# Kernel optimization log

Hardware: AMD Instinct MI355X
Metric: run time of the kernel (lower is better)

Reference implementation:

```python
import jax, jax.numpy as jnp
import numpy as np

B, N_PER_G, DEG = 128, 1024, 8
N = B * N_PER_G
E = N * DEG
IN_DIM, HID, OUT_DIM = 128, 64, 10
EPS = 1e-5


def _gcn(x, src, dst, ew, W, b, n_nodes):
    # GCNConv with add_self_loops=True, symmetric normalization, edge weights ew in {0,1}
    xw = x @ W                                                 # [N, HID]
    deg = jax.ops.segment_sum(ew, dst, num_segments=n_nodes) + 1.0  # +1 self loop
    dinv = jax.lax.rsqrt(deg)
    norm = dinv[src] * dinv[dst] * ew                          # [E]
    agg = jax.ops.segment_sum(xw[src] * norm[:, None], dst, num_segments=n_nodes)
    return agg + xw * (dinv * dinv)[:, None] + b               # self-loop term + bias


def _bn_relu(x, g, beta):
    # BatchNorm1d training-mode stats over node dim (biased var), then ReLU
    mu = x.mean(0)
    var = ((x - mu) ** 2).mean(0)
    return jax.nn.relu((x - mu) * jax.lax.rsqrt(var + EPS) * g + beta)


def _topk_pool(x, src, dst, ew, p, n_per_g):
    # PyG TopKPooling: score = x.p/||p||, keep top ceil(0.8*n) per graph, x *= tanh(score)
    k = (4 * n_per_g + 4) // 5  # ceil(0.8 * n), static
    score = (x @ p) / jnp.linalg.norm(p)                       # [B*n]
    _, idx = jax.lax.top_k(score.reshape(B, n_per_g), k)       # [B, k] local indices
    perm = (idx + (jnp.arange(B) * n_per_g)[:, None]).reshape(-1)  # [B*k] global
    xs = x[perm] * jnp.tanh(score[perm])[:, None]
    # re-index edges; edges touching dropped nodes get weight 0 (mask, fixed E)
    mapping = jnp.full((B * n_per_g,), -1, jnp.int32).at[perm].set(
        jnp.arange(B * k, dtype=jnp.int32))
    ns, nd = mapping[src], mapping[dst]
    valid = (ns >= 0) & (nd >= 0) & (ew > 0)
    return xs, jnp.where(valid, ns, 0), jnp.where(valid, nd, 0), valid.astype(x.dtype), k


def _readout(x, k):
    xg = x.reshape(B, k, HID)
    return jnp.concatenate([xg.mean(1), xg.max(1)], axis=1)    # [B, 2*HID]


def _forward(x, edge_index, W1, b1, gamma1, beta1, p1, W2, b2, gamma2, beta2, p2,
             W3, b3, gamma3, beta3, p3, Wm, bm):
    src, dst = edge_index[0], edge_index[1]
    ew = jnp.ones((E,), x.dtype)
    n = N_PER_G
    blocks = [(W1, b1, gamma1, beta1, p1),
              (W2, b2, gamma2, beta2, p2),
              (W3, b3, gamma3, beta3, p3)]
    readout = jnp.zeros((B, 2 * HID), x.dtype)
    for W, b, g, bt, p in blocks:
        h = _gcn(x, src, dst, ew, W, b, B * n)
        h = _bn_relu(h, g, bt)
        x, src, dst, ew, n = _topk_pool(h, src, dst, ew, p, n)
        readout = readout + _readout(x, n)
    return readout @ Wm + bm                                   # [B, OUT_DIM]


def setup_inputs():
    key = jax.random.key(0)
    ks = jax.random.split(key, 20)
    x = jax.random.normal(ks[0], (N, IN_DIM), jnp.float32)
    src_l = jax.random.randint(ks[1], (E,), 0, N_PER_G)
    dst_l = jax.random.randint(ks[2], (E,), 0, N_PER_G)
    off = jnp.repeat(jnp.arange(B, dtype=jnp.int32) * N_PER_G, N_PER_G * DEG)
    edge_index = jnp.stack([src_l.astype(jnp.int32) + off,
                            dst_l.astype(jnp.int32) + off])   # [2, E] intra-graph
    d = {"x": x, "edge_index": edge_index}
    dims = [(IN_DIM, HID), (HID, HID), (HID, HID)]
    for i, (di, do) in enumerate(dims, 1):
        d[f"W{i}"] = jax.random.normal(ks[3 * i], (di, do), jnp.float32) / np.sqrt(di)
        d[f"b{i}"] = jnp.zeros((do,), jnp.float32)
        d[f"gamma{i}"] = jnp.ones((do,), jnp.float32)
        d[f"beta{i}"] = jnp.zeros((do,), jnp.float32)
        d[f"p{i}"] = jax.random.normal(ks[3 * i + 1], (do,), jnp.float32)
    d["Wm"] = jax.random.normal(ks[15], (2 * HID, OUT_DIM), jnp.float32) / np.sqrt(2 * HID)
    d["bm"] = jnp.zeros((OUT_DIM,), jnp.float32)
    return d


def reference(x, edge_index, W1, b1, gamma1, beta1, p1, W2, b2, gamma2, beta2, p2,
              W3, b3, gamma3, beta3, p3, Wm, bm):
    return _forward(x, edge_index, W1, b1, gamma1, beta1, p1,
                    W2, b2, gamma2, beta2, p2, W3, b3, gamma3, beta3, p3, Wm, bm)
```

## Files before the change

### kernel.cpp

```cpp
#include <hip/hip_runtime.h>
#include <cmath>
#include <cstdint>
#include <cstddef>

#define HID 64
#define NGR 128
#define NTOT 131072
#define EDGES 1048576
#define EPG 8192

__global__ __launch_bounds__(256) void pack_init(
    const int* __restrict__ ei, uint32_t* __restrict__ packed,
    uint16_t* __restrict__ csr_g, uint32_t* __restrict__ rs_g,
    float* __restrict__ dinv_g, float* __restrict__ sums3,
    float* __restrict__ readout) {
  __shared__ int hist[1024];
  __shared__ int part[256];
  __shared__ int cursor[1024];
  int b = blockIdx.x, t = threadIdx.x;
  for (int i = t; i < 1024; i += 256) hist[i] = 0;
  __syncthreads();
  int ebase = b * EPG, nbase = b << 10;
  for (int e = t; e < EPG; e += 256) {
    uint32_t s = (uint32_t)(ei[ebase + e] - nbase);
    uint32_t d = (uint32_t)(ei[EDGES + ebase + e] - nbase);
    packed[ebase + e] = s | (d << 10);
    atomicAdd(&hist[(int)d], 1);
  }
  __syncthreads();
  int h0 = hist[t * 4], h1 = hist[t * 4 + 1], h2 = hist[t * 4 + 2], h3 = hist[t * 4 + 3];
  int tot = h0 + h1 + h2 + h3;
  part[t] = tot;
  __syncthreads();
  for (int off = 1; off < 256; off <<= 1) {
    int v = (t >= off) ? part[t - off] : 0;
    __syncthreads();
    part[t] += v;
    __syncthreads();
  }
  int excl = part[t] - tot;
  int r0 = excl, r1 = r0 + h0, r2 = r1 + h1, r3 = r2 + h2;
  cursor[t * 4 + 0] = r0; cursor[t * 4 + 1] = r1;
  cursor[t * 4 + 2] = r2; cursor[t * 4 + 3] = r3;
  uint32_t* rg = rs_g + b * 1025;
  rg[t * 4 + 0] = r0; rg[t * 4 + 1] = r1; rg[t * 4 + 2] = r2; rg[t * 4 + 3] = r3;
  if (t == 255) rg[1024] = EPG;
  for (int i = t; i < 1024; i += 256)
    dinv_g[(b << 10) + i] = rsqrtf((float)hist[i] + 1.0f);
  __syncthreads();
  for (int e = t; e < EPG; e += 256) {
    uint32_t pk = packed[ebase + e];
    int d = (pk >> 10) & 1023;
    int idx = atomicAdd(&cursor[d], 1);
    csr_g[ebase + idx] = (uint16_t)(pk & 1023);
  }
  if (b < 3 && t < 128) sums3[b * 128 + t] = 0.0f;
  if (t < 128) readout[b * 128 + t] = 0.0f;
}

template<int DIN, bool TIN>
__global__ __launch_bounds__(256) void gemm_xw(
    const float* __restrict__ X, const float* __restrict__ W,
    float* __restrict__ XWT, int n_nodes) {
  __shared__ float sW[32 * HID];
  __shared__ float sX[32 * 132];
  const int t = threadIdx.x;
  const int cq = t & 15, ng = t >> 4;
  const int c4 = cq * 4;
  const int node0 = blockIdx.x * 128;
  const size_t Nn = (size_t)n_nodes;
  float acc[8][4];
#pragma unroll
  for (int n = 0; n < 8; n++) { acc[n][0]=0.f; acc[n][1]=0.f; acc[n][2]=0.f; acc[n][3]=0.f; }

  for (int k0 = 0; k0 < DIN; k0 += 32) {
    ((float4*)sW)[t * 2 + 0] = ((const float4*)(W + (size_t)k0 * HID))[t * 2 + 0];
    ((float4*)sW)[t * 2 + 1] = ((const float4*)(W + (size_t)k0 * HID))[t * 2 + 1];
    if (TIN) {
#pragma unroll
      for (int it = 0; it < 4; it++) {
        int slot = t + it * 256;
        int row = slot >> 5, col4 = (slot & 31) * 4;
        *(float4*)(sX + row * 132 + col4) =
            *(const float4*)(X + (size_t)(k0 + row) * Nn + node0 + col4);
      }
    } else {
      int i4 = (t & 7) * 4;
      int nl = t >> 3;
#pragma unroll
      for (int rep = 0; rep < 4; rep++) {
        int nn = nl + rep * 32;
        float4 v = *(const float4*)(X + (size_t)(node0 + nn) * DIN + k0 + i4);
        sX[(i4 + 0) * 132 + nn] = v.x;
        sX[(i4 + 1) * 132 + nn] = v.y;
        sX[(i4 + 2) * 132 + nn] = v.z;
        sX[(i4 + 3) * 132 + nn] = v.w;
      }
    }
    __syncthreads();
#pragma unroll 4
    for (int i = 0; i < 32; i++) {
      float4 w = *(const float4*)(sW + i * HID + c4);
      const float* xr = sX + i * 132 + ng * 8;
      float4 xa = *(const float4*)xr;
      float4 xb = *(const float4*)(xr + 4);
      float xn[8] = {xa.x, xa.y, xa.z, xa.w, xb.x, xb.y, xb.z, xb.w};
#pragma unroll
      for (int n = 0; n < 8; n++) {
        acc[n][0] = fmaf(xn[n], w.x, acc[n][0]);
        acc[n][1] = fmaf(xn[n], w.y, acc[n][1]);
        acc[n][2] = fmaf(xn[n], w.z, acc[n][2]);
        acc[n][3] = fmaf(xn[n], w.w, acc[n][3]);
      }
    }
    __syncthreads();
  }
#pragma unroll
  for (int cc = 0; cc < 4; cc++) {
    int row = c4 + cc;
    float* o = XWT + (size_t)row * Nn + node0 + ng * 8;
    *(float4*)(o + 0) = make_float4(acc[0][cc], acc[1][cc], acc[2][cc], acc[3][cc]);
    *(float4*)(o + 4) = make_float4(acc[4][cc], acc[5][cc], acc[6][cc], acc[7][cc]);
  }
}

__global__ __launch_bounds__(1024, 8) void edge_agg(
    const uint16_t* __restrict__ csr_g, const uint32_t* __restrict__ rs_g,
    const float* __restrict__ dinv_g, const float* __restrict__ xwT,
    const float* __restrict__ bias, float* __restrict__ hT,
    float* __restrict__ sums) {
  __shared__ float xws[8 * 1028];
  __shared__ float dv[1024];
  __shared__ uint32_t rs[1025];
  __shared__ uint16_t csr_s[8192];
  __shared__ float sredS[16][8], sredQ[16][8];
  const int g = blockIdx.x & 127;
  const int q = blockIdx.x >> 7;
  const int c0 = q * 8;
  const int t = threadIdx.x;
  const int gbase = g << 10;

  dv[t] = dinv_g[gbase + t];
  if (t < 1024) rs[t] = rs_g[g * 1025 + t];
  if (t == 0) rs[1024] = EPG;
  ((uint4*)csr_s)[t] = ((const uint4*)(csr_g + (size_t)g * EPG))[t];
  for (int slot = t; slot < 2048; slot += 1024) {
    int c = slot >> 8, pos4 = (slot & 255) * 4;
    float4 v = *(const float4*)(xwT + (size_t)(c0 + c) * NTOT + gbase + pos4);
    float4 dd = *(const float4*)(dinv_g + gbase + pos4);
    v.x *= dd.x; v.y *= dd.y; v.z *= dd.z; v.w *= dd.w;
    *(float4*)(xws + c * 1028 + pos4) = v;
  }
  __syncthreads();

  const int c = t & 7, j = t >> 3;
  const float* xc = xws + c * 1028;
  const float bv = bias[c0 + c];
  float* hrow = hT + (size_t)(c0 + c) * NTOT + gbase;
  float S = 0.0f, Q = 0.0f;
  for (int d = j; d < 1024; d += 128) {
    float dvd = dv[d];
    if (dvd == 0.0f) continue;
    int e = rs[d], e1 = rs[d + 1];
    float a0 = 0.0f, a1 = 0.0f;
    for (; e + 2 <= e1; e += 2) {
      int s0 = csr_s[e], s1 = csr_s[e + 1];
      a0 += xc[s0];
      a1 += xc[s1];
    }
    if (e < e1) a0 += xc[csr_s[e]];
    float hv = (a0 + a1 + xc[d]) * dvd + bv;
    hrow[d] = hv;
    S += hv; Q += hv * hv;
  }
#pragma unroll
  for (int m = 8; m < 64; m <<= 1) { S += __shfl_xor(S, m); Q += __shfl_xor(Q, m); }
  {
    int lane = t & 63, w = t >> 6;
    if (lane < 8) { sredS[w][lane] = S; sredQ[w][lane] = Q; }
  }
  __syncthreads();
  if (t < 8) {
    float a = 0.0f;
    for (int w2 = 0; w2 < 16; w2++) a += sredS[w2][t];
    atomicAdd(&sums[c0 + t], a);
  } else if (t < 16) {
    int cc = t - 8;
    float a = 0.0f;
    for (int w2 = 0; w2 < 16; w2++) a += sredQ[w2][cc];
    atomicAdd(&sums[64 + cc + c0], a);
  }
}

__global__ __launch_bounds__(256) void score_kernel(
    const float* __restrict__ hT, const float* __restrict__ sums,
    const float* __restrict__ gamma, const float* __restrict__ beta,
    const float* __restrict__ p, const float* __restrict__ dinv_g,
    float* __restrict__ score, float* __restrict__ stanh_g, float inv_n) {
  __shared__ float ssc[64], ssh[64], sp[64];
  __shared__ float sipn;
  int b = blockIdx.x >> 2, seg = (blockIdx.x & 3) << 8;
  int t = threadIdx.x;
  int node = (b << 10) + seg + t;
  if (t < 64) {
    float mu = sums[t] * inv_n;
    float var = fmaxf(sums[64 + t] * inv_n - mu * mu, 0.0f);
    float sc = rsqrtf(var + 1e-5f) * gamma[t];
    ssc[t] = sc; ssh[t] = beta[t] - mu * sc;
    sp[t] = p[t];
  }
  __syncthreads();
  if (t == 0) {
    float s = 0.0f;
    for (int i = 0; i < 64; i++) s += sp[i] * sp[i];
    sipn = rsqrtf(s);
  }
  __syncthreads();
  const float* hp = hT + node;
  float s0 = 0.0f;
#pragma unroll 16
  for (int c = 0; c < 64; c++) {
    float y = fmaxf(fmaf(hp[(size_t)c * NTOT], ssc[c], ssh[c]), 0.0f);
    s0 = fmaf(y, sp[c], s0);
  }
  float v0 = s0 * sipn;
  score[node] = (dinv_g[node] > 0.0f) ? v0 : -INFINITY;
  stanh_g[node] = tanhf(v0);
}

__global__ __launch_bounds__(1024) void topk_kernel(
    const float* __restrict__ score, const uint32_t* __restrict__ packed,
    float* __restrict__ dinv_g, int* __restrict__ snext_g, int k, int hasNext) {
  __shared__ float __align__(16) ssc[1024];
  __shared__ int snext[1024];
  __shared__ int shist[1024];
  int b = blockIdx.x, t = threadIdx.x;
  int gbase = b << 10;
  ssc[t] = score[gbase + t];
  shist[t] = 0;
  __syncthreads();
  float my = ssc[t];
  int r = 0;
  for (int jb = 0; jb < 256; jb++) {
    float4 v = ((const float4*)ssc)[jb];
    int j0 = jb * 4;
    r += (v.x > my) || (v.x == my && (j0 + 0) < t);
    r += (v.y > my) || (v.y == my && (j0 + 1) < t);
    r += (v.z > my) || (v.z == my && (j0 + 2) < t);
    r += (v.w > my) || (v.w == my && (j0 + 3) < t);
  }
  int kept = (r < k) ? 1 : 0;
  snext[t] = kept;
  snext_g[gbase + t] = kept;
  __syncthreads();
  if (hasNext) {
    const uint32_t* pe = packed + (size_t)b * EPG;
#pragma unroll
    for (int e0 = 0; e0 < EPG; e0 += 1024) {
      uint32_t pk = pe[e0 + t];
      int s = pk & 1023, d = (pk >> 10) & 1023;
      if (snext[s] & snext[d]) atomicAdd(&shist[d], 1);
    }
    __syncthreads();
    dinv_g[gbase + t] = kept ? rsqrtf((float)shist[t] + 1.0f) : 0.0f;
  }
}

__global__ __launch_bounds__(256) void pool_kernel(
    const float* __restrict__ hT, const float* __restrict__ sums,
    const float* __restrict__ gamma, const float* __restrict__ beta,
    const float* __restrict__ stanh_g, const int* __restrict__ snext_g,
    float* __restrict__ xT_out, float* __restrict__ readout,
    int k, float inv_n) {
  __shared__ float ssc[64], ssh[64];
  __shared__ float sth[1024];
  __shared__ int skn[1024];
  __shared__ float redS[4][8], redM[4][8];
  int g = blockIdx.x & 127, q = blockIdx.x >> 7;
  int t = threadIdx.x;
  int gbase = g << 10;
  if (t < 64) {
    float mu = sums[t] * inv_n;
    float var = fmaxf(sums[64 + t] * inv_n - mu * mu, 0.0f);
    float sc = rsqrtf(var + 1e-5f) * gamma[t];
    ssc[t] = sc; ssh[t] = beta[t] - mu * sc;
  }
  for (int i = t; i < 1024; i += 256) {
    sth[i] = stanh_g[gbase + i];
    skn[i] = snext_g[gbase + i];
  }
  __syncthreads();
  int lane = t & 63, w = t >> 6;
#pragma unroll
  for (int i = 0; i < 8; i++) {
    int c = q * 8 + i;
    const float* hrow = hT + (size_t)c * NTOT + gbase;
    float* xrow = xT_out ? (xT_out + (size_t)c * NTOT + gbase) : nullptr;
    float scc = ssc[c], shh = ssh[c];
    float S = 0.0f, M = -INFINITY;
    for (int nd = t; nd < 1024; nd += 256) {
      bool kn = skn[nd] != 0;
      float y = fmaxf(fmaf(hrow[nd], scc, shh), 0.0f) * sth[nd];
      y = kn ? y : 0.0f;
      if (xrow) xrow[nd] = y;
      S += y;
      if (kn) M = fmaxf(M, y);
    }
#pragma unroll
    for (int m = 1; m < 64; m <<= 1) {
      S += __shfl_xor(S, m);
      M = fmaxf(M, __shfl_xor(M, m));
    }
    if (lane == 0) { redS[w][i] = S; redM[w][i] = M; }
  }
  __syncthreads();
  if (t < 8) {
    float S = redS[0][t] + redS[1][t] + redS[2][t] + redS[3][t];
    readout[g * 128 + q * 8 + t] += S / (float)k;
  } else if (t < 16) {
    int i = t - 8;
    float M = fmaxf(fmaxf(redM[0][i], redM[1][i]), fmaxf(redM[2][i], redM[3][i]));
    readout[g * 128 + 64 + q * 8 + i] += M;
  }
}

__global__ __launch_bounds__(256) void final_linear(
    const float* __restrict__ readout, const float* __restrict__ Wm,
    const float* __restrict__ bm, float* __restrict__ out) {
  int idx = blockIdx.x * 256 + threadIdx.x;
  if (idx >= NGR * 10) return;
  int b = idx / 10, o = idx - b * 10;
  float acc = bm[o];
  const float* r = readout + (size_t)b * 128;
  for (int c = 0; c < 128; c++) acc = fmaf(r[c], Wm[c * 10 + o], acc);
  out[idx] = acc;
}

extern "C" void kernel_launch(void* const* d_in, const int* in_sizes, int n_in,
                              void* d_out, int out_size, void* d_ws, size_t ws_size,
                              hipStream_t stream) {
  (void)in_sizes; (void)n_in; (void)out_size; (void)ws_size;
  const float* x  = (const float*)d_in[0];
  const int*   ei = (const int*)d_in[1];
  const float* Wk[3]  = {(const float*)d_in[2],  (const float*)d_in[7],  (const float*)d_in[12]};
  const float* bk[3]  = {(const float*)d_in[3],  (const float*)d_in[8],  (const float*)d_in[13]};
  const float* gk[3]  = {(const float*)d_in[4],  (const float*)d_in[9],  (const float*)d_in[14]};
  const float* btk[3] = {(const float*)d_in[5],  (const float*)d_in[10], (const float*)d_in[15]};
  const float* pk[3]  = {(const float*)d_in[6],  (const float*)d_in[11], (const float*)d_in[16]};
  const float* Wm = (const float*)d_in[17];
  const float* bm = (const float*)d_in[18];
  float* out = (float*)d_out;

  float* ws = (float*)d_ws;
  size_t off = 0;
  auto alloc = [&](size_t nfl) {
    float* ptr = ws + off;
    off += (nfl + 63) & ~(size_t)63;
    return ptr;
  };
  float* bufXW = alloc((size_t)NTOT * 64);
  float* bufH  = alloc((size_t)NTOT * 64);
  float* bufX  = alloc((size_t)NTOT * 64);
  float* dinv_g = alloc(NTOT);
  float* score  = alloc(NTOT);
  float* stanh_g = alloc(NTOT);
  int*   snext_g = (int*)alloc(NTOT);
  uint32_t* packed = (uint32_t*)alloc(EDGES);
  uint16_t* csr    = (uint16_t*)alloc(EDGES / 2);
  uint32_t* rs     = (uint32_t*)alloc(NGR * 1025);
  float* sums3 = alloc(3 * 128);
  float* readout = alloc(NGR * 2 * HID);

  pack_init<<<NGR, 256, 0, stream>>>(ei, packed, csr, rs, dinv_g, sums3, readout);

  const int   kk[3] = {820, 656, 525};
  const float invn[3] = {1.0f / (float)NTOT, 1.0f / (float)(NGR * 820),
                         1.0f / (float)(NGR * 656)};

  for (int L = 0; L < 3; L++) {
    float* sums = sums3 + L * 128;
    if (L == 0)
      gemm_xw<128, false><<<NTOT / 128, 256, 0, stream>>>(x, Wk[0], bufXW, NTOT);
    else
      gemm_xw<64, true><<<NTOT / 128, 256, 0, stream>>>(bufX, Wk[L], bufXW, NTOT);
    edge_agg<<<8 * NGR, 1024, 0, stream>>>(csr, rs, dinv_g, bufXW, bk[L], bufH, sums);
    score_kernel<<<4 * NGR, 256, 0, stream>>>(bufH, sums, gk[L], btk[L], pk[L],
                                              dinv_g, score, stanh_g, invn[L]);
    topk_kernel<<<NGR, 1024, 0, stream>>>(score, packed, dinv_g, snext_g,
                                          kk[L], (L < 2) ? 1 : 0);
    pool_kernel<<<8 * NGR, 256, 0, stream>>>(bufH, sums, gk[L], btk[L],
                                             stanh_g, snext_g,
                                             (L < 2) ? bufX : nullptr, readout,
                                             kk[L], invn[L]);
  }
  final_linear<<<5, 256, 0, stream>>>(readout, Wm, bm, out);
}
```

Before: 529.0 us.

## Split top-k ranking across four blocks per graph and move degree recompute into pooling

The top-k rank computation now runs on four blocks per graph. Each thread compares one node against a quarter of the scores, and the partial counts are combined with shuffles, so each block does less serial work and more blocks run at once. The next layer's degree and dinv computation moves out of topk_kernel into pool_kernel. There it walks the per-destination CSR rows and counts kept neighbours instead of running shared-memory atomics over the packed edge list. The cost is that the score array is loaded and staged four times per graph, and pool_kernel gains an uneven per-row loop.

After: 486.4 us. -8.0%, faster.

```diff
diff --git a/kernel.cpp b/kernel.cpp
--- a/kernel.cpp
+++ b/kernel.cpp
@@ -229,49 +229,41 @@
 }
 
 __global__ __launch_bounds__(1024) void topk_kernel(
-    const float* __restrict__ score, const uint32_t* __restrict__ packed,
-    float* __restrict__ dinv_g, int* __restrict__ snext_g, int k, int hasNext) {
-  __shared__ float __align__(16) ssc[1024];
-  __shared__ int snext[1024];
-  __shared__ int shist[1024];
-  int b = blockIdx.x, t = threadIdx.x;
+    const float* __restrict__ score, int* __restrict__ snext_g, int k) {
+  __shared__ float __align__(16) ssc2[4 * 260];
+  int b = blockIdx.x >> 2, p = blockIdx.x & 3;
+  int t = threadIdx.x;
   int gbase = b << 10;
-  ssc[t] = score[gbase + t];
-  shist[t] = 0;
-  __syncthreads();
-  float my = ssc[t];
+  float sv = score[gbase + t];
+  ssc2[(t >> 8) * 260 + (t & 255)] = sv;
+  __syncthreads();
+  int il = t >> 2, jq = t & 3;
+  int gi = p * 256 + il;
+  float my = ssc2[(gi >> 8) * 260 + (gi & 255)];
+  const float4* base = (const float4*)(ssc2 + jq * 260);
+  int jbase = jq * 256;
   int r = 0;
-  for (int jb = 0; jb < 256; jb++) {
-    float4 v = ((const float4*)ssc)[jb];
-    int j0 = jb * 4;
-    r += (v.x > my) || (v.x == my && (j0 + 0) < t);
-    r += (v.y > my) || (v.y == my && (j0 + 1) < t);
-    r += (v.z > my) || (v.z == my && (j0 + 2) < t);
-    r += (v.w > my) || (v.w == my && (j0 + 3) < t);
-  }
-  int kept = (r < k) ? 1 : 0;
-  snext[t] = kept;
-  snext_g[gbase + t] = kept;
-  __syncthreads();
-  if (hasNext) {
-    const uint32_t* pe = packed + (size_t)b * EPG;
-#pragma unroll
-    for (int e0 = 0; e0 < EPG; e0 += 1024) {
-      uint32_t pk = pe[e0 + t];
-      int s = pk & 1023, d = (pk >> 10) & 1023;
-      if (snext[s] & snext[d]) atomicAdd(&shist[d], 1);
-    }
-    __syncthreads();
-    dinv_g[gbase + t] = kept ? rsqrtf((float)shist[t] + 1.0f) : 0.0f;
-  }
+#pragma unroll 8
+  for (int m = 0; m < 64; m++) {
+    float4 v = base[m];
+    int j0 = jbase + m * 4;
+    r += (v.x > my) || (v.x == my && (j0 + 0) < gi);
+    r += (v.y > my) || (v.y == my && (j0 + 1) < gi);
+    r += (v.z > my) || (v.z == my && (j0 + 2) < gi);
+    r += (v.w > my) || (v.w == my && (j0 + 3) < gi);
+  }
+  r += __shfl_xor(r, 1);
+  r += __shfl_xor(r, 2);
+  if (jq == 0) snext_g[gbase + gi] = (r < k) ? 1 : 0;
 }
 
 __global__ __launch_bounds__(256) void pool_kernel(
     const float* __restrict__ hT, const float* __restrict__ sums,
     const float* __restrict__ gamma, const float* __restrict__ beta,
     const float* __restrict__ stanh_g, const int* __restrict__ snext_g,
-    float* __restrict__ xT_out, float* __restrict__ readout,
-    int k, float inv_n) {
+    const uint16_t* __restrict__ csr_g, const uint32_t* __restrict__ rs_g,
+    float* __restrict__ xT_out, float* __restrict__ dinv_g,
+    float* __restrict__ readout, int k, float inv_n, int hasNext) {
   __shared__ float ssc[64], ssh[64];
   __shared__ float sth[1024];
   __shared__ int skn[1024];
@@ -312,6 +304,18 @@
       M = fmaxf(M, __shfl_xor(M, m));
     }
     if (lane == 0) { redS[w][i] = S; redM[w][i] = M; }
+  }
+  if (hasNext && t < 128) {
+    int d = q * 128 + t;
+    if (skn[d]) {
+      uint32_t e0 = rs_g[g * 1025 + d], e1 = rs_g[g * 1025 + d + 1];
+      const uint16_t* row = csr_g + (size_t)g * EPG;
+      int cnt = 0;
+      for (uint32_t e = e0; e < e1; e++) cnt += skn[row[e]];
+      dinv_g[gbase + d] = rsqrtf((float)cnt + 1.0f);
+    } else {
+      dinv_g[gbase + d] = 0.0f;
+    }
   }
   __syncthreads();
   if (t < 8) {
@@ -386,12 +390,12 @@
     edge_agg<<<8 * NGR, 1024, 0, stream>>>(csr, rs, dinv_g, bufXW, bk[L], bufH, sums);
     score_kernel<<<4 * NGR, 256, 0, stream>>>(bufH, sums, gk[L], btk[L], pk[L],
                                               dinv_g, score, stanh_g, invn[L]);
-    topk_kernel<<<NGR, 1024, 0, stream>>>(score, packed, dinv_g, snext_g,
-                                          kk[L], (L < 2) ? 1 : 0);
+    topk_kernel<<<4 * NGR, 1024, 0, stream>>>(score, snext_g, kk[L]);
     pool_kernel<<<8 * NGR, 256, 0, stream>>>(bufH, sums, gk[L], btk[L],
-                                             stanh_g, snext_g,
-                                             (L < 2) ? bufX : nullptr, readout,
-                                             kk[L], invn[L]);
+                                             stanh_g, snext_g, csr, rs,
+                                             (L < 2) ? bufX : nullptr, dinv_g,
+                                             readout, kk[L], invn[L],
+                                             (L < 2) ? 1 : 0);
   }
   final_linear<<<5, 256, 0, stream>>>(readout, Wm, bm, out);
 }
```
